# Performance work log

Measured on AMD Instinct MI355X. Metric: run time of the kernel, lower is better.

The kernel has to match this reference:

```python
import jax, jax.numpy as jnp
import numpy as np

N_NODES = 50000
N_EDGES = 800000
EPS = 1e-12  # F.normalize default eps


def spmm(edge_row, edge_col, edge_val, dense):
    # sparse [N,N] (COO edges) @ dense [N,D] -> [N,D]
    gathered = edge_val[:, None] * dense[edge_col]          # [E, D]
    return jax.ops.segment_sum(gathered, edge_row, num_segments=N_NODES)


def setup_inputs() -> dict:
    key = jax.random.key(0)
    ks = jax.random.split(key, 8)
    x = jax.random.normal(ks[0], (N_NODES, 300), dtype=jnp.float32)
    edge_row = jax.random.randint(ks[1], (N_EDGES,), 0, N_NODES, dtype=jnp.int32)
    edge_col = jax.random.randint(ks[2], (N_EDGES,), 0, N_NODES, dtype=jnp.int32)
    edge_val = jax.random.uniform(ks[3], (N_EDGES,), dtype=jnp.float32)
    W1 = jax.random.normal(ks[4], (256, 300), dtype=jnp.float32) * 0.05
    b1 = jax.random.normal(ks[5], (256,), dtype=jnp.float32) * 0.05
    W2 = jax.random.normal(ks[6], (128, 256), dtype=jnp.float32) * 0.05
    b2 = jax.random.normal(ks[7], (128,), dtype=jnp.float32) * 0.05
    return {"x": x, "edge_row": edge_row, "edge_col": edge_col,
            "edge_val": edge_val, "W1": W1, "b1": b1, "W2": W2, "b2": b2}


def reference(x, edge_row, edge_col, edge_val, W1, b1, W2, b2):
    # GraphConv 1: X @ W1.T, SpMM with adj, +bias, ReLU (dropout is eval no-op)
    h = x @ W1.T                                            # [N, 256]
    h = spmm(edge_row, edge_col, edge_val, h) + b1
    h = jax.nn.relu(h)
    # GraphConv last: no ReLU
    h = h @ W2.T                                            # [N, 128]
    h = spmm(edge_row, edge_col, edge_val, h) + b2
    # F.normalize(x): row-wise L2 normalize with eps clamp
    norm = jnp.linalg.norm(h, axis=1, keepdims=True)
    return h / jnp.maximum(norm, EPS)
```

## Files before the change

kernel.cpp:

```cpp
#include <hip/hip_runtime.h>
#include <math.h>

#define NN 50000
#define NE 800000
#define ESLICE2 400128

typedef __bf16 bf16x8 __attribute__((ext_vector_type(8)));
typedef __bf16 bf16x4 __attribute__((ext_vector_type(4)));
typedef float f32x4 __attribute__((ext_vector_type(4)));

__device__ __forceinline__ void gload16(const void* g, void* l){
  __builtin_amdgcn_global_load_lds((const __attribute__((address_space(1))) void*)g,
                                   (__attribute__((address_space(3))) void*)l, 16, 0, 0);
}


__global__ __launch_bounds__(256)
void conv_all(const float* __restrict__ x, const float* __restrict__ W1,
              const float* __restrict__ W2, __bf16* __restrict__ xb,
              __bf16* __restrict__ W1b, __bf16* __restrict__ W2b,
              int* __restrict__ cur){
  const int b = blockIdx.x;
  if (b >= 15752){
    const int i = (b - 15752) * 256 + threadIdx.x;
    if (i < NN) cur[i] = 0;
    return;
  }
  const float* src; __bf16* dst; int q, M, K, Kp;
  if (b < 15640){ src = x;  dst = xb;  q = b * 256 + threadIdx.x; M = NN;  K = 300; Kp = 320; }
  else if (b < 15720){ src = W1; dst = W1b; q = (b - 15640) * 256 + threadIdx.x; M = 256; K = 300; Kp = 320; }
  else { src = W2; dst = W2b; q = (b - 15720) * 256 + threadIdx.x; M = 128; K = 256; Kp = 256; }
  const int perRow = Kp >> 2;
  const int r = q / perRow;
  const int k = (q - r * perRow) << 2;
  float4 v = make_float4(0.f, 0.f, 0.f, 0.f);
  if (r < M && k < K) v = *(const float4*)(src + (size_t)r * K + k);
  bf16x4 o;
  o[0] = (__bf16)v.x; o[1] = (__bf16)v.y; o[2] = (__bf16)v.z; o[3] = (__bf16)v.w;
  *(bf16x4*)(dst + (size_t)r * Kp + k) = o;
}


__global__ __launch_bounds__(256)
void k_rank(const int* __restrict__ erow, int* __restrict__ cnt, int* __restrict__ pos){
  const int t = blockIdx.x * 256 + threadIdx.x;
  #pragma unroll
  for (int k = 0; k < 2; ++k){
    const int e = t + k * ESLICE2;
    if (e < NE){
      const int r = erow[e];
      pos[e] = atomicAdd(&cnt[r], 1);
    }
  }
}

__global__ __launch_bounds__(256)
void k_scan1(const int* __restrict__ cnt, int* __restrict__ rs, int* __restrict__ part, int n){
  const int t = threadIdx.x, b = blockIdx.x;
  const int i = b * 256 + t;
  int v = (i < n) ? cnt[i] : 0;
  const int lane = t & 63, w = t >> 6;
  int s = v;
  #pragma unroll
  for (int d = 1; d < 64; d <<= 1){ int u = __shfl_up(s, d); if (lane >= d) s += u; }
  __shared__ int wsum[4];
  if (lane == 63) wsum[w] = s;
  __syncthreads();
  int add = 0;
  #pragma unroll
  for (int k = 0; k < 4; ++k) if (k < w) add += wsum[k];
  s += add;
  if (i < n) rs[i + 1] = s;
  if (t == 255) part[b] = s;
}

__global__ __launch_bounds__(256)
void k_scan3(int* __restrict__ rs, const int* __restrict__ part, int n){
  const int t = threadIdx.x, b = blockIdx.x;
  int v = (t < b) ? part[t] : 0;
  const int lane = t & 63, w = t >> 6;
  #pragma unroll
  for (int m = 32; m; m >>= 1) v += __shfl_xor(v, m);
  __shared__ int wsum[4];
  if (lane == 0) wsum[w] = v;
  __syncthreads();
  const int add = wsum[0] + wsum[1] + wsum[2] + wsum[3];
  const int i = b * 256 + t;
  if (i < n) rs[i + 1] += add;
  if (b == 0 && t == 0) rs[0] = 0;
}

__global__ __launch_bounds__(256)
void k_scatter2(const int* __restrict__ erow, const int* __restrict__ ecol,
                const float* __restrict__ evalv, const int* __restrict__ rs,
                const int* __restrict__ pos, int2* __restrict__ out){
  const int t = blockIdx.x * 256 + threadIdx.x;
  #pragma unroll
  for (int k = 0; k < 2; ++k){
    const int e = t + k * ESLICE2;
    if (e < NE){
      const int r = erow[e];
      const int p = rs[r] + pos[e];
      out[p] = make_int2(ecol[e], __float_as_int(evalv[e]));
    }
  }
}


template<int KT, int LGN>
__global__ __launch_bounds__(256)
void gemm_bf16(const __bf16* __restrict__ A, const __bf16* __restrict__ B,
               __bf16* __restrict__ C, int ld, int N){
  __shared__ char ldsbuf[49152];
  const int tid = threadIdx.x;
  const int lane = tid & 63;
  const int L = blockIdx.x;
  const int bmt = (L & 7) + ((L >> (3 + LGN)) << 3);
  if (bmt >= 391) return;
  const int bm = bmt * 128;
  const int bn = ((L >> 3) & ((1 << LGN) - 1)) * 64;
  const int wr = (tid >> 7) & 1;
  const int wc = (tid >> 6) & 1;

  f32x4 acc[4][2];
  #pragma unroll
  for (int i = 0; i < 4; ++i)
    #pragma unroll
    for (int j = 0; j < 2; ++j) acc[i][j] = (f32x4){0.f, 0.f, 0.f, 0.f};

  auto stage = [&](int kt, int sel){
    char* lb = ldsbuf + sel * 24576;
    #pragma unroll
    for (int i = 0; i < 4; ++i){
      const int d = i * 4096 + tid * 16;
      const int row = d >> 7;
      const int colb = (d & 127) ^ ((row & 7) << 4);
      const __bf16* gp = A + (size_t)(bm + row) * ld + kt * 64 + (colb >> 1);
      gload16(gp, lb + i * 4096 + (tid & 192) * 16);
    }
    #pragma unroll
    for (int i = 0; i < 2; ++i){
      const int d = i * 4096 + tid * 16;
      const int row = d >> 7;
      const int colb = (d & 127) ^ ((row & 7) << 4);
      const __bf16* gp = B + (size_t)(bn + row) * ld + kt * 64 + (colb >> 1);
      gload16(gp, lb + 16384 + i * 4096 + (tid & 192) * 16);
    }
  };

  auto compute = [&](int sel){
    const char* lA = ldsbuf + sel * 24576;
    const char* lB = lA + 16384;
    #pragma unroll
    for (int c = 0; c < 2; ++c){
      bf16x8 av[4], bv[2];
      #pragma unroll
      for (int i = 0; i < 4; ++i){
        const int row = wr * 64 + i * 16 + (lane & 15);
        const int colb = (c * 64 + ((lane >> 4) << 4)) ^ ((row & 7) << 4);
        av[i] = *(const bf16x8*)(lA + row * 128 + colb);
      }
      #pragma unroll
      for (int j = 0; j < 2; ++j){
        const int row = wc * 32 + j * 16 + (lane & 15);
        const int colb = (c * 64 + ((lane >> 4) << 4)) ^ ((row & 7) << 4);
        bv[j] = *(const bf16x8*)(lB + row * 128 + colb);
      }
      #pragma unroll
      for (int i = 0; i < 4; ++i)
        #pragma unroll
        for (int j = 0; j < 2; ++j)
          acc[i][j] = __builtin_amdgcn_mfma_f32_16x16x32_bf16(av[i], bv[j], acc[i][j], 0, 0, 0);
    }
  };

  stage(0, 0);
  for (int kt = 0; kt < KT; ++kt){
    __syncthreads();
    if (kt + 1 < KT) stage(kt + 1, (kt + 1) & 1);
    compute(kt & 1);
  }

  __syncthreads();
  float* lw = (float*)ldsbuf;
  #pragma unroll
  for (int i = 0; i < 4; ++i)
    #pragma unroll
    for (int j = 0; j < 2; ++j)
      #pragma unroll
      for (int r = 0; r < 4; ++r){
        const int row = wr * 64 + i * 16 + ((lane >> 4) << 2) + r;
        const int col = wc * 32 + j * 16 + (lane & 15);
        lw[row * 68 + col] = acc[i][j][r];
      }
  __syncthreads();
  #pragma unroll
  for (int p = 0; p < 4; ++p){
    const int row = p * 32 + (tid >> 3);
    const int col8 = (tid & 7) * 8;
    const float4 v0 = *(const float4*)&lw[row * 68 + col8];
    const float4 v1 = *(const float4*)&lw[row * 68 + col8 + 4];
    bf16x8 o;
    o[0] = (__bf16)v0.x; o[1] = (__bf16)v0.y; o[2] = (__bf16)v0.z; o[3] = (__bf16)v0.w;
    o[4] = (__bf16)v1.x; o[5] = (__bf16)v1.y; o[6] = (__bf16)v1.z; o[7] = (__bf16)v1.w;
    *(bf16x8*)(C + (size_t)(bm + row) * N + bn + col8) = o;
  }
}


__global__ __launch_bounds__(256)
void spmm_relu_half(const int2* __restrict__ ecv, const int* __restrict__ start,
                    const __bf16* __restrict__ H, const float* __restrict__ bias,
                    __bf16* __restrict__ out, int ch0){
  const int w = (blockIdx.x * 256 + threadIdx.x) >> 6;
  const int lane = threadIdx.x & 63;
  const int quar = lane >> 4, sl = lane & 15;
  if (w >= NN) return;
  const int s = start[w], e = start[w + 1];
  float a[8];
  #pragma unroll
  for (int k = 0; k < 8; ++k) a[k] = 0.f;
  for (int base = s; base < e; base += 64){
    int2 cv = make_int2(0, 0);
    if (base + lane < e) cv = ecv[base + lane];
    const int m = min(64, e - base);
    for (int j2 = 0; 16 * j2 < m; ++j2){
      int cc[4]; float vv[4];
      #pragma unroll
      for (int u = 0; u < 4; ++u){
        const int idx = 16 * j2 + quar + 4 * u;
        cc[u] = __shfl(cv.x, idx);
        vv[u] = __int_as_float(__shfl(cv.y, idx));
        if (idx >= m){ cc[u] = 0; vv[u] = 0.f; }
      }
      bf16x8 h[4];
      #pragma unroll
      for (int u = 0; u < 4; ++u)
        h[u] = *(const bf16x8*)(H + (size_t)cc[u] * 256 + ch0 + sl * 8);
      #pragma unroll
      for (int u = 0; u < 4; ++u)
        #pragma unroll
        for (int k = 0; k < 8; ++k) a[k] = fmaf(vv[u], (float)h[u][k], a[k]);
    }
  }
  #pragma unroll
  for (int k = 0; k < 8; ++k){
    a[k] += __shfl_xor(a[k], 32);
    a[k] += __shfl_xor(a[k], 16);
  }
  const float4 b0 = *(const float4*)(bias + ch0 + sl * 8);
  const float4 b1 = *(const float4*)(bias + ch0 + sl * 8 + 4);
  bf16x8 o;
  o[0] = (__bf16)fmaxf(a[0] + b0.x, 0.f);
  o[1] = (__bf16)fmaxf(a[1] + b0.y, 0.f);
  o[2] = (__bf16)fmaxf(a[2] + b0.z, 0.f);
  o[3] = (__bf16)fmaxf(a[3] + b0.w, 0.f);
  o[4] = (__bf16)fmaxf(a[4] + b1.x, 0.f);
  o[5] = (__bf16)fmaxf(a[5] + b1.y, 0.f);
  o[6] = (__bf16)fmaxf(a[6] + b1.z, 0.f);
  o[7] = (__bf16)fmaxf(a[7] + b1.w, 0.f);
  if (quar == 0) *(bf16x8*)(out + (size_t)w * 256 + ch0 + sl * 8) = o;
}

__global__ __launch_bounds__(256)
void spmm_bias_norm_b16(const int2* __restrict__ ecv, const int* __restrict__ start,
                        const __bf16* __restrict__ H, const float* __restrict__ bias,
                        float* __restrict__ out){
  const int w = (blockIdx.x * 256 + threadIdx.x) >> 6;
  const int lane = threadIdx.x & 63;
  const int quar = lane >> 4, sl = lane & 15;
  if (w >= NN) return;
  const int s = start[w], e = start[w + 1];
  float a[8];
  #pragma unroll
  for (int k = 0; k < 8; ++k) a[k] = 0.f;
  for (int base = s; base < e; base += 64){
    int2 cv = make_int2(0, 0);
    if (base + lane < e) cv = ecv[base + lane];
    const int m = min(64, e - base);
    for (int j2 = 0; 16 * j2 < m; ++j2){
      int cc[4]; float vv[4];
      #pragma unroll
      for (int u = 0; u < 4; ++u){
        const int idx = 16 * j2 + quar + 4 * u;
        cc[u] = __shfl(cv.x, idx);
        vv[u] = __int_as_float(__shfl(cv.y, idx));
        if (idx >= m){ cc[u] = 0; vv[u] = 0.f; }
      }
      bf16x8 h[4];
      #pragma unroll
      for (int u = 0; u < 4; ++u)
        h[u] = *(const bf16x8*)(H + (size_t)cc[u] * 128 + sl * 8);
      #pragma unroll
      for (int u = 0; u < 4; ++u)
        #pragma unroll
        for (int k = 0; k < 8; ++k) a[k] = fmaf(vv[u], (float)h[u][k], a[k]);
    }
  }
  #pragma unroll
  for (int k = 0; k < 8; ++k){
    a[k] += __shfl_xor(a[k], 32);
    a[k] += __shfl_xor(a[k], 16);
  }
  const float4 b0 = *(const float4*)(bias + sl * 8);
  const float4 b1 = *(const float4*)(bias + sl * 8 + 4);
  float f[8];
  f[0] = a[0] + b0.x; f[1] = a[1] + b0.y; f[2] = a[2] + b0.z; f[3] = a[3] + b0.w;
  f[4] = a[4] + b1.x; f[5] = a[5] + b1.y; f[6] = a[6] + b1.z; f[7] = a[7] + b1.w;
  float ss = 0.f;
  #pragma unroll
  for (int k = 0; k < 8; ++k) ss = fmaf(f[k], f[k], ss);
  #pragma unroll
  for (int m2 = 1; m2 < 16; m2 <<= 1) ss += __shfl_xor(ss, m2);
  const float inv = 1.f / fmaxf(sqrtf(ss), 1e-12f);
  if (quar == 0){
    float4 o0 = make_float4(f[0] * inv, f[1] * inv, f[2] * inv, f[3] * inv);
    float4 o1 = make_float4(f[4] * inv, f[5] * inv, f[6] * inv, f[7] * inv);
    *(float4*)(out + (size_t)w * 128 + sl * 8) = o0;
    *(float4*)(out + (size_t)w * 128 + sl * 8 + 4) = o1;
  }
}


extern "C" void kernel_launch(void* const* d_in, const int* in_sizes, int n_in,
                              void* d_out, int out_size, void* d_ws, size_t ws_size,
                              hipStream_t stream){
  const float* x    = (const float*)d_in[0];
  const int*   erow = (const int*)d_in[1];
  const int*   ecol = (const int*)d_in[2];
  const float* evalv= (const float*)d_in[3];
  const float* W1   = (const float*)d_in[4];
  const float* b1   = (const float*)d_in[5];
  const float* W2   = (const float*)d_in[6];
  const float* b2   = (const float*)d_in[7];
  float* out = (float*)d_out;

  char* ws = (char*)d_ws;
  __bf16* xb  = (__bf16*)(ws);
  __bf16* W1b = (__bf16*)(ws + 32030720);
  __bf16* W2b = (__bf16*)(ws + 32194560);
  __bf16* h1  = (__bf16*)(ws + 32260096);
  __bf16* h2  = (__bf16*)(ws + 57884672);
  __bf16* h3  = (__bf16*)(ws + 83509248);
  int2*   ecv = (int2*)(ws + 96321536);
  int*    rs  = (int*)(ws + 102721536);
  int*    part= (int*)(ws + 102921552);
  int*    cur = (int*)(ws + 102922368);
  int*    pos = (int*)(ws + 32260096);

  conv_all<<<15948, 256, 0, stream>>>(x, W1, W2, xb, W1b, W2b, cur);

  k_rank<<<1563, 256, 0, stream>>>(erow, cur, pos);
  k_scan1<<<196, 256, 0, stream>>>(cur, rs, part, NN);
  k_scan3<<<196, 256, 0, stream>>>(rs, part, NN);
  k_scatter2<<<1563, 256, 0, stream>>>(erow, ecol, evalv, rs, pos, ecv);

  gemm_bf16<5, 2><<<1568, 256, 0, stream>>>(xb, W1b, h1, 320, 256);
  spmm_relu_half<<<12500, 256, 0, stream>>>(ecv, rs, h1, b1, h2, 0);
  spmm_relu_half<<<12500, 256, 0, stream>>>(ecv, rs, h1, b1, h2, 128);

  gemm_bf16<4, 1><<<784, 256, 0, stream>>>(h2, W2b, h3, 256, 128);
  spmm_bias_norm_b16<<<12500, 256, 0, stream>>>(ecv, rs, h3, b2, out);
}
```

Measured before the change: 190.6 us.

## Merge independent preprocessing kernels into combined launches to cut launch gaps

Folds the edge-rank atomic pass into the bf16 conversion kernel, folds the CSR scatter into the first GEMM launch, and merges the two half-channel SpMM launches into one grid. A separate tiny kernel now zeroes the counters, and the pos buffer moves to its own workspace region so it no longer aliases h1, which the GEMM writes in the same launch. The goal is fewer kernel launches and idle tail gaps, with independent work sharing one grid. In exchange the heterogeneous blocks in each fused grid may balance poorly, and scat_gemm reserves 48 KB of LDS even for scatter blocks, which can limit occupancy.

```diff
diff --git a/kernel.cpp b/kernel.cpp
--- a/kernel.cpp
+++ b/kernel.cpp
@@ -16,20 +16,35 @@
 
 
 __global__ __launch_bounds__(256)
-void conv_all(const float* __restrict__ x, const float* __restrict__ W1,
-              const float* __restrict__ W2, __bf16* __restrict__ xb,
-              __bf16* __restrict__ W1b, __bf16* __restrict__ W2b,
-              int* __restrict__ cur){
+void k_zero(int* __restrict__ p){
+  const int i = blockIdx.x * 256 + threadIdx.x;
+  if (i < NN) p[i] = 0;
+}
+
+
+__global__ __launch_bounds__(256)
+void rank_conv(const int* __restrict__ erow, int* __restrict__ cnt, int* __restrict__ pos,
+               const float* __restrict__ x, const float* __restrict__ W1,
+               const float* __restrict__ W2, __bf16* __restrict__ xb,
+               __bf16* __restrict__ W1b, __bf16* __restrict__ W2b){
   const int b = blockIdx.x;
-  if (b >= 15752){
-    const int i = (b - 15752) * 256 + threadIdx.x;
-    if (i < NN) cur[i] = 0;
+  if (b < 1563){
+    const int t = b * 256 + threadIdx.x;
+    #pragma unroll
+    for (int k = 0; k < 2; ++k){
+      const int e = t + k * ESLICE2;
+      if (e < NE){
+        const int r = erow[e];
+        pos[e] = atomicAdd(&cnt[r], 1);
+      }
+    }
     return;
   }
+  const int cb = b - 1563;
   const float* src; __bf16* dst; int q, M, K, Kp;
-  if (b < 15640){ src = x;  dst = xb;  q = b * 256 + threadIdx.x; M = NN;  K = 300; Kp = 320; }
-  else if (b < 15720){ src = W1; dst = W1b; q = (b - 15640) * 256 + threadIdx.x; M = 256; K = 300; Kp = 320; }
-  else { src = W2; dst = W2b; q = (b - 15720) * 256 + threadIdx.x; M = 128; K = 256; Kp = 256; }
+  if (cb < 15640){ src = x;  dst = xb;  q = cb * 256 + threadIdx.x; M = NN;  K = 300; Kp = 320; }
+  else if (cb < 15720){ src = W1; dst = W1b; q = (cb - 15640) * 256 + threadIdx.x; M = 256; K = 300; Kp = 320; }
+  else { src = W2; dst = W2b; q = (cb - 15720) * 256 + threadIdx.x; M = 128; K = 256; Kp = 256; }
   const int perRow = Kp >> 2;
   const int r = q / perRow;
   const int k = (q - r * perRow) << 2;
@@ -42,19 +57,6 @@
 
 
 __global__ __launch_bounds__(256)
-void k_rank(const int* __restrict__ erow, int* __restrict__ cnt, int* __restrict__ pos){
-  const int t = blockIdx.x * 256 + threadIdx.x;
-  #pragma unroll
-  for (int k = 0; k < 2; ++k){
-    const int e = t + k * ESLICE2;
-    if (e < NE){
-      const int r = erow[e];
-      pos[e] = atomicAdd(&cnt[r], 1);
-    }
-  }
-}
-
-__global__ __launch_bounds__(256)
 void k_scan1(const int* __restrict__ cnt, int* __restrict__ rs, int* __restrict__ part, int n){
   const int t = threadIdx.x, b = blockIdx.x;
   const int i = b * 256 + t;
@@ -90,19 +92,120 @@
   if (b == 0 && t == 0) rs[0] = 0;
 }
 
-__global__ __launch_bounds__(256)
-void k_scatter2(const int* __restrict__ erow, const int* __restrict__ ecol,
-                const float* __restrict__ evalv, const int* __restrict__ rs,
-                const int* __restrict__ pos, int2* __restrict__ out){
-  const int t = blockIdx.x * 256 + threadIdx.x;
-  #pragma unroll
-  for (int k = 0; k < 2; ++k){
-    const int e = t + k * ESLICE2;
-    if (e < NE){
-      const int r = erow[e];
-      const int p = rs[r] + pos[e];
-      out[p] = make_int2(ecol[e], __float_as_int(evalv[e]));
-    }
+
+template<int KT, int LGN>
+__global__ __launch_bounds__(256)
+void scat_gemm(const int* __restrict__ erow, const int* __restrict__ ecol,
+               const float* __restrict__ evalv, const int* __restrict__ rs,
+               const int* __restrict__ pos, int2* __restrict__ ecv,
+               const __bf16* __restrict__ A, const __bf16* __restrict__ B,
+               __bf16* __restrict__ C, int ld, int N){
+  __shared__ char ldsbuf[49152];
+  const int tid = threadIdx.x;
+  if (blockIdx.x < 1563){
+    const int t = blockIdx.x * 256 + tid;
+    #pragma unroll
+    for (int k = 0; k < 2; ++k){
+      const int e = t + k * ESLICE2;
+      if (e < NE){
+        const int r = erow[e];
+        const int p = rs[r] + pos[e];
+        ecv[p] = make_int2(ecol[e], __float_as_int(evalv[e]));
+      }
+    }
+    return;
+  }
+  const int lane = tid & 63;
+  const int L = blockIdx.x - 1563;
+  const int bmt = (L & 7) + ((L >> (3 + LGN)) << 3);
+  if (bmt >= 391) return;
+  const int bm = bmt * 128;
+  const int bn = ((L >> 3) & ((1 << LGN) - 1)) * 64;
+  const int wr = (tid >> 7) & 1;
+  const int wc = (tid >> 6) & 1;
+
+  f32x4 acc[4][2];
+  #pragma unroll
+  for (int i = 0; i < 4; ++i)
+    #pragma unroll
+    for (int j = 0; j < 2; ++j) acc[i][j] = (f32x4){0.f, 0.f, 0.f, 0.f};
+
+  auto stage = [&](int kt, int sel){
+    char* lb = ldsbuf + sel * 24576;
+    #pragma unroll
+    for (int i = 0; i < 4; ++i){
+      const int d = i * 4096 + tid * 16;
+      const int row = d >> 7;
+      const int colb = (d & 127) ^ ((row & 7) << 4);
+      const __bf16* gp = A + (size_t)(bm + row) * ld + kt * 64 + (colb >> 1);
+      gload16(gp, lb + i * 4096 + (tid & 192) * 16);
+    }
+    #pragma unroll
+    for (int i = 0; i < 2; ++i){
+      const int d = i * 4096 + tid * 16;
+      const int row = d >> 7;
+      const int colb = (d & 127) ^ ((row & 7) << 4);
+      const __bf16* gp = B + (size_t)(bn + row) * ld + kt * 64 + (colb >> 1);
+      gload16(gp, lb + 16384 + i * 4096 + (tid & 192) * 16);
+    }
+  };
+
+  auto compute = [&](int sel){
+    const char* lA = ldsbuf + sel * 24576;
+    const char* lB = lA + 16384;
+    #pragma unroll
+    for (int c = 0; c < 2; ++c){
+      bf16x8 av[4], bv[2];
+      #pragma unroll
+      for (int i = 0; i < 4; ++i){
+        const int row = wr * 64 + i * 16 + (lane & 15);
+        const int colb = (c * 64 + ((lane >> 4) << 4)) ^ ((row & 7) << 4);
+        av[i] = *(const bf16x8*)(lA + row * 128 + colb);
+      }
+      #pragma unroll
+      for (int j = 0; j < 2; ++j){
+        const int row = wc * 32 + j * 16 + (lane & 15);
+        const int colb = (c * 64 + ((lane >> 4) << 4)) ^ ((row & 7) << 4);
+        bv[j] = *(const bf16x8*)(lB + row * 128 + colb);
+      }
+      #pragma unroll
+      for (int i = 0; i < 4; ++i)
+        #pragma unroll
+        for (int j = 0; j < 2; ++j)
+          acc[i][j] = __builtin_amdgcn_mfma_f32_16x16x32_bf16(av[i], bv[j], acc[i][j], 0, 0, 0);
+    }
+  };
+
+  stage(0, 0);
+  for (int kt = 0; kt < KT; ++kt){
+    __syncthreads();
+    if (kt + 1 < KT) stage(kt + 1, (kt + 1) & 1);
+    compute(kt & 1);
+  }
+
+  __syncthreads();
+  float* lw = (float*)ldsbuf;
+  #pragma unroll
+  for (int i = 0; i < 4; ++i)
+    #pragma unroll
+    for (int j = 0; j < 2; ++j)
+      #pragma unroll
+      for (int r = 0; r < 4; ++r){
+        const int row = wr * 64 + i * 16 + ((lane >> 4) << 2) + r;
+        const int col = wc * 32 + j * 16 + (lane & 15);
+        lw[row * 68 + col] = acc[i][j][r];
+      }
+  __syncthreads();
+  #pragma unroll
+  for (int p = 0; p < 4; ++p){
+    const int row = p * 32 + (tid >> 3);
+    const int col8 = (tid & 7) * 8;
+    const float4 v0 = *(const float4*)&lw[row * 68 + col8];
+    const float4 v1 = *(const float4*)&lw[row * 68 + col8 + 4];
+    bf16x8 o;
+    o[0] = (__bf16)v0.x; o[1] = (__bf16)v0.y; o[2] = (__bf16)v0.z; o[3] = (__bf16)v0.w;
+    o[4] = (__bf16)v1.x; o[5] = (__bf16)v1.y; o[6] = (__bf16)v1.z; o[7] = (__bf16)v1.w;
+    *(bf16x8*)(C + (size_t)(bm + row) * N + bn + col8) = o;
   }
 }
 
@@ -209,10 +312,13 @@
 
 
 __global__ __launch_bounds__(256)
-void spmm_relu_half(const int2* __restrict__ ecv, const int* __restrict__ start,
-                    const __bf16* __restrict__ H, const float* __restrict__ bias,
-                    __bf16* __restrict__ out, int ch0){
-  const int w = (blockIdx.x * 256 + threadIdx.x) >> 6;
+void spmm_relu_b16(const int2* __restrict__ ecv, const int* __restrict__ start,
+                   const __bf16* __restrict__ H, const float* __restrict__ bias,
+                   __bf16* __restrict__ out){
+  const int half = (blockIdx.x >= 12500) ? 1 : 0;
+  const int bb = blockIdx.x - half * 12500;
+  const int ch0 = half * 128;
+  const int w = (bb * 256 + threadIdx.x) >> 6;
   const int lane = threadIdx.x & 63;
   const int quar = lane >> 4, sl = lane & 15;
   if (w >= NN) return;
@@ -346,19 +452,15 @@
   int*    rs  = (int*)(ws + 102721536);
   int*    part= (int*)(ws + 102921552);
   int*    cur = (int*)(ws + 102922368);
-  int*    pos = (int*)(ws + 32260096);
-
-  conv_all<<<15948, 256, 0, stream>>>(x, W1, W2, xb, W1b, W2b, cur);
-
-  k_rank<<<1563, 256, 0, stream>>>(erow, cur, pos);
+  int*    pos = (int*)(ws + 103122368);
+
+  k_zero<<<196, 256, 0, stream>>>(cur);
+  rank_conv<<<17315, 256, 0, stream>>>(erow, cur, pos, x, W1, W2, xb, W1b, W2b);
   k_scan1<<<196, 256, 0, stream>>>(cur, rs, part, NN);
   k_scan3<<<196, 256, 0, stream>>>(rs, part, NN);
-  k_scatter2<<<1563, 256, 0, stream>>>(erow, ecol, evalv, rs, pos, ecv);
-
-  gemm_bf16<5, 2><<<1568, 256, 0, stream>>>(xb, W1b, h1, 320, 256);
-  spmm_relu_half<<<12500, 256, 0, stream>>>(ecv, rs, h1, b1, h2, 0);
-  spmm_relu_half<<<12500, 256, 0, stream>>>(ecv, rs, h1, b1, h2, 128);
-
+  scat_gemm<5, 2><<<3131, 256, 0, stream>>>(erow, ecol, evalv, rs, pos, ecv,
+                                            xb, W1b, h1, 320, 256);
+  spmm_relu_b16<<<25000, 256, 0, stream>>>(ecv, rs, h1, b1, h2);
   gemm_bf16<4, 1><<<784, 256, 0, stream>>>(h2, W2b, h3, 256, 128);
   spmm_bias_norm_b16<<<12500, 256, 0, stream>>>(ecv, rs, h3, b2, out);
 }
```

Measured after the change: 181.9 us. -4.6%, faster.
